# Kernel tuning notes

Hardware: AMD Instinct MI355X
Metric: run time of the kernel (lower is better)

## Reference

```python
import jax, jax.numpy as jnp
import numpy as np

B = 256                       # graphs in batch
NS = [4096, 2048, 1024, 512]  # nodes per graph at each stage (pool halves)
F_IN = 3                      # num_feature
D = 64                        # dim_cell
EPB = [32768, 16384, 8192]    # edges per graph at each layer (deg ~8)
NEG = 0.2                     # GATConv leaky_relu negative slope
EPS = 1e-5                    # BatchNorm eps
L = 3                         # layer_cell


def setup_inputs() -> dict:
    key = jax.random.key(0)
    ks = jax.random.split(key, 16)
    inp = {"x": jax.random.normal(ks[0], (B * NS[0], F_IN), jnp.float32)}
    dims = [F_IN, D, D]
    for i in range(L):
        inp[f"W{i}"] = jax.random.normal(ks[1 + i], (dims[i], D), jnp.float32) / np.sqrt(dims[i]).astype(np.float32)
        inp[f"as{i}"] = jax.random.normal(ks[4 + i], (D,), jnp.float32) * 0.1
        inp[f"ad{i}"] = jax.random.normal(ks[7 + i], (D,), jnp.float32) * 0.1
        inp[f"b{i}"] = jnp.zeros((D,), jnp.float32)
        inp[f"e{i}"] = jax.random.randint(ks[10 + i], (2, EPB[i]), 0, NS[i], jnp.int32)
        # cluster assignment: merge node pairs -> every cluster id occupied
        inp[f"c{i}"] = (jnp.arange(NS[i], dtype=jnp.int32) // 2)
    return inp


def _tile_edges(edge, n_per_graph):
    # replicate per-graph edge list across batch with node offsets, then add self-loops
    offs = (jnp.arange(B, dtype=edge.dtype) * n_per_graph)
    e = (edge[:, None, :] + offs[None, :, None]).reshape(2, -1)  # [2, B*E]
    loops = jnp.arange(B * n_per_graph, dtype=edge.dtype)
    return jnp.concatenate([e, jnp.stack([loops, loops])], axis=1)


def _gat(x, W, a_src, a_dst, bias, edge, n_tot):
    # PyG GATConv, heads=1: shared linear, edge-softmax over incoming edges
    h = x @ W                                # [n_tot, D]
    al_s = h @ a_src                         # [n_tot]
    al_d = h @ a_dst
    src, dst = edge[0], edge[1]              # message src j -> target i
    e = jax.nn.leaky_relu(al_s[src] + al_d[dst], NEG)
    m = jax.ops.segment_max(e, dst, num_segments=n_tot)
    ex = jnp.exp(e - m[dst])
    z = jax.ops.segment_sum(ex, dst, num_segments=n_tot)
    alpha = ex / z[dst]                      # softmax per target node
    out = jax.ops.segment_sum(alpha[:, None] * h[src], dst, num_segments=n_tot)
    return out + bias


def reference(x, W0, as0, ad0, b0, W1, as1, ad1, b1, W2, as2, ad2, b2,
              e0, e1, e2, c0, c1, c2):
    Ws, As, Ad, Bs = [W0, W1, W2], [as0, as1, as2], [ad0, ad1, ad2], [b0, b1, b2]
    Es, Cs = [e0, e1, e2], [c0, c1, c2]
    h = x
    for i in range(L):
        n_tot = B * NS[i]
        edge = _tile_edges(Es[i], NS[i])
        h = jax.nn.relu(_gat(h, Ws[i], As[i], Ad[i], Bs[i], edge, n_tot))
        # cluster max_pool: scatter-max nodes into clusters, offset per graph
        c_out = NS[i + 1]
        seg = (Cs[i][None, :] + (jnp.arange(B, dtype=jnp.int32) * c_out)[:, None]).reshape(-1)
        h = jax.ops.segment_max(h, seg, num_segments=B * c_out)
        # BatchNorm1d(affine=False), training-mode batch statistics
        h = (h - h.mean(axis=0)) * jax.lax.rsqrt(h.var(axis=0) + EPS)
    return h.reshape(B, NS[L] * D)
```

## Files before the change

kernel.cpp:

```cpp
#include <hip/hip_runtime.h>
#include <stdint.h>

#define NEG_SLOPE 0.2f
#define BN_EPS 1e-5f

typedef unsigned short u16;
typedef unsigned int   u32;
typedef __attribute__((ext_vector_type(2))) float  v2f;
typedef __attribute__((ext_vector_type(4))) float  f32x4;
typedef __attribute__((ext_vector_type(8))) short  short8;

__device__ __forceinline__ float lrelu(float x){ return fmaxf(x, NEG_SLOPE*x); }
__device__ __forceinline__ float bf2f(u16 u){ return __uint_as_float(((u32)u) << 16); }
__device__ __forceinline__ u16 f2bf(float f){
  u32 u = __float_as_uint(f);
  return (u16)((u + 0x7fffu + ((u >> 16) & 1u)) >> 16);
}

__global__ __launch_bounds__(256) void init_k(int* __restrict__ counts, u16* __restrict__ s0,
                                              u16* __restrict__ s1, u16* __restrict__ s2,
                                              int nc, int n0, int n1, int n2){
  int t = blockIdx.x*256 + threadIdx.x;
  int y = blockIdx.y;
  if (y==0){ if (t<nc) counts[t]=0; }
  else {
    u16* sd = (y==1)?s0:(y==2)?s1:s2;
    int n   = (y==1)?n0:(y==2)?n1:n2;
    if (t<n) sd[t]=0xFFFFu;
  }
}

__global__ __launch_bounds__(256) void hist_all_k(const int* __restrict__ el0, const int* __restrict__ el1,
                                                  const int* __restrict__ el2, int* __restrict__ c0,
                                                  int* __restrict__ c1, int* __restrict__ c2,
                                                  int n0, int n1, int n2){
  int t = blockIdx.x*256 + threadIdx.x;
  int L = blockIdx.y;
  const int* dst = (L==0)?(el0+n0):(L==1)?(el1+n1):(el2+n2);
  int* counts    = (L==0)?c0:(L==1)?c1:c2;
  int n          = (L==0)?n0:(L==1)?n1:n2;
  if (t < n) atomicAdd(&counts[dst[t]], 1);
}

__global__ __launch_bounds__(1024) void scan_all_k(int* __restrict__ c0, int* __restrict__ c1, int* __restrict__ c2,
                         int* __restrict__ ip0, int* __restrict__ ip1, int* __restrict__ ip2,
                         int* __restrict__ cu0, int* __restrict__ cu1, int* __restrict__ cu2,
                         u16* __restrict__ sd0, u16* __restrict__ sd1, u16* __restrict__ sd2,
                         int n0, int n1, int n2){
  int L = blockIdx.x;
  const int* counts = (L==0)?c0:(L==1)?c1:c2;
  int* indptr2      = (L==0)?ip0:(L==1)?ip1:ip2;
  int* cursor       = (L==0)?cu0:(L==1)?cu1:cu2;
  u16* ell_src      = (L==0)?sd0:(L==1)?sd1:sd2;
  int n             = (L==0)?n0:(L==1)?n1:n2;
  __shared__ int part[1024];
  int tid = threadIdx.x;
  int base = tid*4;
  int v0=0,v1=0,v2=0,v3=0;
  if (base+0<n) v0 = (counts[base+0]+4)&~3;
  if (base+1<n) v1 = (counts[base+1]+4)&~3;
  if (base+2<n) v2 = (counts[base+2]+4)&~3;
  if (base+3<n) v3 = (counts[base+3]+4)&~3;
  part[tid] = v0+v1+v2+v3;
  __syncthreads();
  for (int off=1; off<1024; off<<=1){
    int t2 = (tid>=off)?part[tid-off]:0;
    __syncthreads();
    part[tid] += t2;
    __syncthreads();
  }
  int run = (tid>0)?part[tid-1]:0;
  if (base+0<n){ indptr2[base+0]=run; cursor[base+0]=run+1; ell_src[run]=(u16)(base+0); run+=v0; }
  if (base+1<n){ indptr2[base+1]=run; cursor[base+1]=run+1; ell_src[run]=(u16)(base+1); run+=v1; }
  if (base+2<n){ indptr2[base+2]=run; cursor[base+2]=run+1; ell_src[run]=(u16)(base+2); run+=v2; }
  if (base+3<n){ indptr2[base+3]=run; cursor[base+3]=run+1; ell_src[run]=(u16)(base+3); run+=v3; }
  if (tid==0) indptr2[n] = part[1023];
}

__global__ __launch_bounds__(256) void scatter_all_k(const int* __restrict__ el0, const int* __restrict__ el1,
                         const int* __restrict__ el2, int* __restrict__ cu0, int* __restrict__ cu1,
                         int* __restrict__ cu2, u16* __restrict__ sd0, u16* __restrict__ sd1,
                         u16* __restrict__ sd2, int n0, int n1, int n2){
  int t = blockIdx.x*256 + threadIdx.x;
  int L = blockIdx.y;
  const int* el = (L==0)?el0:(L==1)?el1:el2;
  int* cursor   = (L==0)?cu0:(L==1)?cu1:cu2;
  u16* ell_src  = (L==0)?sd0:(L==1)?sd1:sd2;
  int n         = (L==0)?n0:(L==1)?n1:n2;
  if (t < n){
    int dd = el[n + t];
    int p = atomicAdd(&cursor[dd], 1);
    ell_src[p] = (u16)el[t];
  }
}

__global__ __launch_bounds__(1024) void pairsort_k(const int* __restrict__ c0, const int* __restrict__ c1,
                         const int* __restrict__ c2, u16* __restrict__ pm0, u16* __restrict__ pm1,
                         u16* __restrict__ pm2, int np0, int np1, int np2){
  int L = blockIdx.x;
  const int* counts = (L==0)?c0:(L==1)?c1:c2;
  u16* perm = (L==0)?pm0:(L==1)?pm1:pm2;
  int np    = (L==0)?np0:(L==1)?np1:np2;
  __shared__ int hist[64];
  __shared__ int pos[64];
  int t = threadIdx.x;
  if (t < 64) hist[t] = 0;
  __syncthreads();
  for (int p=t; p<np; p+=1024){
    int k = min(max(counts[2*p], counts[2*p+1]), 63);
    atomicAdd(&hist[k], 1);
  }
  __syncthreads();
  if (t == 0){ int run=0; for (int i=0;i<64;i++){ pos[i]=run; run+=hist[i]; } }
  __syncthreads();
  for (int p=t; p<np; p+=1024){
    int k = min(max(counts[2*p], counts[2*p+1]), 63);
    int q = atomicAdd(&pos[k], 1);
    perm[q] = (u16)p;
  }
}

__global__ __launch_bounds__(256) void gemm3_k(const float* __restrict__ x, const float* __restrict__ Wg,
                        const float* __restrict__ asrc, const float* __restrict__ adst,
                        u16* __restrict__ h, float* __restrict__ als, float* __restrict__ ald, int nrows8)
{
  const int l = threadIdx.x & 63;
  const int g = l >> 3;
  const int o = l & 7;
  float W0[8], W1[8], W2[8];
  float vs0=0.f,vs1=0.f,vs2=0.f,vd0=0.f,vd1=0.f,vd2=0.f;
  #pragma unroll
  for (int j=0;j<8;j++){
    W0[j] = Wg[      o*8 + j];
    W1[j] = Wg[ 64 + o*8 + j];
    W2[j] = Wg[128 + o*8 + j];
    float as = asrc[o*8 + j], ad = adst[o*8 + j];
    vs0 = fmaf(W0[j], as, vs0); vs1 = fmaf(W1[j], as, vs1); vs2 = fmaf(W2[j], as, vs2);
    vd0 = fmaf(W0[j], ad, vd0); vd1 = fmaf(W1[j], ad, vd1); vd2 = fmaf(W2[j], ad, vd2);
  }
  #pragma unroll
  for (int off=1; off<8; off<<=1){
    vs0 += __shfl_xor(vs0,off); vs1 += __shfl_xor(vs1,off); vs2 += __shfl_xor(vs2,off);
    vd0 += __shfl_xor(vd0,off); vd1 += __shfl_xor(vd1,off); vd2 += __shfl_xor(vd2,off);
  }
  int wv = blockIdx.x*4 + (int)(threadIdx.x>>6);
  int stride = gridDim.x*4;
  for (int blk = wv; blk < nrows8; blk += stride){
    int r = blk*8 + g;
    float x0 = x[(size_t)r*3+0];
    float x1 = x[(size_t)r*3+1];
    float x2 = x[(size_t)r*3+2];
    u32 pk[4];
    #pragma unroll
    for (int j=0;j<8;j+=2){
      float a0 = fmaf(x0, W0[j],   fmaf(x1, W1[j],   x2*W2[j]));
      float a1 = fmaf(x0, W0[j+1], fmaf(x1, W1[j+1], x2*W2[j+1]));
      pk[j>>1] = (u32)f2bf(a0) | ((u32)f2bf(a1) << 16);
    }
    ((int4*)(h + ((size_t)r << 6)))[o] = make_int4((int)pk[0],(int)pk[1],(int)pk[2],(int)pk[3]);
    if (o == 0){
      als[r] = fmaf(x2, vs2, fmaf(x1, vs1, x0*vs0));
      ald[r] = fmaf(x2, vd2, fmaf(x1, vd1, x0*vd0));
    }
  }
}

__global__ __launch_bounds__(128) void prep_w_k(const float* __restrict__ W, const float* __restrict__ asrc,
                        const float* __restrict__ adst, const float* __restrict__ scratch, float invN,
                        u16* __restrict__ wswz, float* __restrict__ cvec){
  __shared__ float mean_s[64], rstd_s[64], vs_s[64], vd_s[64], cv_s[64], acc[128];
  int t = threadIdx.x;
  float s = 0.f;
  #pragma unroll 8
  for (int b2=0;b2<256;b2++) s += scratch[b2*128 + t];
  acc[t] = s;
  __syncthreads();
  if (t < 64){
    float m = acc[t]*invN;
    float var = acc[64+t]*invN - m*m;
    mean_s[t] = m; rstd_s[t] = rsqrtf(var + BN_EPS);
  }
  __syncthreads();
  if (t < 64){
    float c = 0.f;
    for (int k=0;k<64;k++) c = fmaf(mean_s[k]*rstd_s[k], W[k*64+t], c);
    cv_s[t] = c; cvec[t] = c;
    float vs = 0.f, vd = 0.f;
    for (int col=0; col<64; col++){
      float wv = W[t*64+col];
      vs = fmaf(wv, asrc[col], vs);
      vd = fmaf(wv, adst[col], vd);
    }
    vs_s[t] = rstd_s[t]*vs; vd_s[t] = rstd_s[t]*vd;
  }
  __syncthreads();
  if (t == 0){
    float cs=0.f, cd=0.f;
    for (int col=0; col<64; col++){ cs = fmaf(cv_s[col], asrc[col], cs); cd = fmaf(cv_s[col], adst[col], cd); }
    cvec[64] = cs; cvec[65] = cd;
  }
  if (t < 64){
    #pragma unroll
    for (int f=0; f<8; f++){
      int tt = f >> 1, ch = f & 1;
      #pragma unroll
      for (int j=0; j<8; j++){
        int k   = ch*32 + (t>>4)*8 + j;
        int col = tt*16 + (t&15);
        wswz[(f*64 + t)*8 + j] = f2bf(rstd_s[k] * W[k*64 + col]);
      }
    }
    #pragma unroll
    for (int f=8; f<10; f++){
      int ch = f - 8;
      #pragma unroll
      for (int j=0; j<8; j++){
        int k = ch*32 + (t>>4)*8 + j;
        int colp = t & 15;
        float val = (colp==0)? vs_s[k] : (colp==1)? vd_s[k] : 0.f;
        wswz[(f*64 + t)*8 + j] = f2bf(val);
      }
    }
  }
}

__global__ __launch_bounds__(256) void gemm64_mfma_k(const u16* __restrict__ Pin, const u16* __restrict__ wswz,
                        const float* __restrict__ cvec,
                        u16* __restrict__ h, float* __restrict__ als, float* __restrict__ ald, int nblk16)
{
  const int l = threadIdx.x & 63;
  const int q = l >> 4;
  const int c = l & 15;
  short8 B[10];
  const int4* wsw = (const int4*)wswz;
  #pragma unroll
  for (int f=0; f<10; f++){
    int4 v = wsw[f*64 + l];
    B[f] = *(short8*)&v;
  }
  float cl[4];
  #pragma unroll
  for (int t=0;t<4;t++) cl[t] = cvec[t*16+c];
  const float const_s = cvec[64], const_d = cvec[65];
  int gw = blockIdx.x*4 + (int)(threadIdx.x>>6);
  int stride = gridDim.x*4;
  for (int blk = gw; blk < nblk16; blk += stride){
    size_t rowbase = (size_t)blk*16;
    const int4* arow = (const int4*)(Pin + (rowbase + c)*64);
    int4 a0v = arow[q];
    int4 a1v = arow[4+q];
    short8 A0 = *(short8*)&a0v, A1 = *(short8*)&a1v;
    f32x4 C0={0.f,0.f,0.f,0.f}, C1=C0, C2=C0, C3=C0, C4=C0;
    C0 = __builtin_amdgcn_mfma_f32_16x16x32_bf16(A0, B[0], C0, 0,0,0);
    C0 = __builtin_amdgcn_mfma_f32_16x16x32_bf16(A1, B[1], C0, 0,0,0);
    C1 = __builtin_amdgcn_mfma_f32_16x16x32_bf16(A0, B[2], C1, 0,0,0);
    C1 = __builtin_amdgcn_mfma_f32_16x16x32_bf16(A1, B[3], C1, 0,0,0);
    C2 = __builtin_amdgcn_mfma_f32_16x16x32_bf16(A0, B[4], C2, 0,0,0);
    C2 = __builtin_amdgcn_mfma_f32_16x16x32_bf16(A1, B[5], C2, 0,0,0);
    C3 = __builtin_amdgcn_mfma_f32_16x16x32_bf16(A0, B[6], C3, 0,0,0);
    C3 = __builtin_amdgcn_mfma_f32_16x16x32_bf16(A1, B[7], C3, 0,0,0);
    C4 = __builtin_amdgcn_mfma_f32_16x16x32_bf16(A0, B[8], C4, 0,0,0);
    C4 = __builtin_amdgcn_mfma_f32_16x16x32_bf16(A1, B[9], C4, 0,0,0);
    #pragma unroll
    for (int t=0;t<4;t++){
      f32x4 C = (t==0)?C0:(t==1)?C1:(t==2)?C2:C3;
      #pragma unroll
      for (int reg=0;reg<4;reg++){
        h[(rowbase + q*4 + reg)*64 + t*16 + c] = f2bf(C[reg] - cl[t]);
      }
    }
    if (c == 0){
      #pragma unroll
      for (int reg=0;reg<4;reg++) als[rowbase + q*4 + reg] = C4[reg] - const_s;
    } else if (c == 1){
      #pragma unroll
      for (int reg=0;reg<4;reg++) ald[rowbase + q*4 + reg] = C4[reg] - const_d;
    }
  }
}

__global__ __launch_bounds__(256) void gat_pool_k(const u16* __restrict__ h, const float* __restrict__ bias,
                      const int* __restrict__ indptr2, const int* __restrict__ counts,
                      const u16* __restrict__ perm, const u16* __restrict__ ell_src,
                      const float* __restrict__ als, const float* __restrict__ ald,
                      u16* __restrict__ P, int log2NS, int nwaves)
{
  const int l = threadIdx.x & 63;
  const int g = l >> 3;
  const int o = l & 7;
  const int NB  = gridDim.x;
  const int bid = blockIdx.x;
  const int lb  = (bid & 7) * (NB >> 3) + (bid >> 3);
  const int wv  = lb * 4 + (int)(threadIdx.x >> 6);
  if (wv >= nwaves) return;

  const int wbits = log2NS - 3;
  const int b    = wv >> wbits;
  const int widx = wv & ((1 << wbits) - 1);
  const int pairslot = widx*4 + (g >> 1);
  const int prow = perm[pairslot];
  const int d = 2*prow + (g & 1);
  const int nmask = (1 << log2NS) - 1;
  const int base = b << log2NS;
  const u32* hb = (const u32*)(h + ((size_t)base << 6)) + (o << 2);
  const float* alsg = als + base;

  const int p0  = indptr2[d];
  const int cnt = counts[d] + 1;
  const float ald_d = ald[base + d];

  const float* bp = bias + (o << 3);
  float4 bA = *(const float4*)(bp);
  float4 bB = *(const float4*)(bp + 4);

  v2f a01={0.f,0.f}, a23={0.f,0.f}, a45={0.f,0.f}, a67={0.f,0.f};
  float z = 0.f;

  int m0 = ell_src[p0];
  int m1 = ell_src[p0+1];
  int m2 = ell_src[p0+2];
  int s0i = m0 & nmask;
  const u32* hp0 = hb + ((size_t)s0i << 5);
  u32 h00=hp0[0], h01=hp0[1], h02=hp0[2], h03=hp0[3];
  float al0 = alsg[s0i];
  int s1i = m1 & nmask;
  const u32* hp1 = hb + ((size_t)s1i << 5);
  u32 h10=hp1[0], h11=hp1[1], h12=hp1[2], h13=hp1[3];
  float al1 = alsg[s1i];

  for (int it = 0; it < cnt; ++it){
    int s2i = m2 & nmask;
    const u32* hp2 = hb + ((size_t)s2i << 5);
    u32 n0=hp2[0], n1=hp2[1], n2=hp2[2], n3=hp2[3];
    float al2 = alsg[s2i];
    int m3 = ell_src[p0 + it + 3];
    float w = (m0 == 0xFFFF) ? 0.f : __expf(lrelu(al0 + ald_d));
    z += w;
    v2f w2 = {w, w};
    a01 += (v2f){ __uint_as_float(h00 << 16), __uint_as_float(h00 & 0xffff0000u) } * w2;
    a23 += (v2f){ __uint_as_float(h01 << 16), __uint_as_float(h01 & 0xffff0000u) } * w2;
    a45 += (v2f){ __uint_as_float(h02 << 16), __uint_as_float(h02 & 0xffff0000u) } * w2;
    a67 += (v2f){ __uint_as_float(h03 << 16), __uint_as_float(h03 & 0xffff0000u) } * w2;
    m0 = m1; m1 = m2; m2 = m3;
    h00=h10; h01=h11; h02=h12; h03=h13; al0 = al1;
    h10=n0;  h11=n1;  h12=n2;  h13=n3;  al1 = al2;
  }

  float rz = __builtin_amdgcn_rcpf(z);
  float q0 = fmaxf(fmaf(a01.x, rz, bA.x), 0.f);
  float q1 = fmaxf(fmaf(a01.y, rz, bA.y), 0.f);
  float q2 = fmaxf(fmaf(a23.x, rz, bA.z), 0.f);
  float q3 = fmaxf(fmaf(a23.y, rz, bA.w), 0.f);
  float q4 = fmaxf(fmaf(a45.x, rz, bB.x), 0.f);
  float q5 = fmaxf(fmaf(a45.y, rz, bB.y), 0.f);
  float q6 = fmaxf(fmaf(a67.x, rz, bB.z), 0.f);
  float q7 = fmaxf(fmaf(a67.y, rz, bB.w), 0.f);
  q0 = fmaxf(q0, __shfl_xor(q0, 8));
  q1 = fmaxf(q1, __shfl_xor(q1, 8));
  q2 = fmaxf(q2, __shfl_xor(q2, 8));
  q3 = fmaxf(q3, __shfl_xor(q3, 8));
  q4 = fmaxf(q4, __shfl_xor(q4, 8));
  q5 = fmaxf(q5, __shfl_xor(q5, 8));
  q6 = fmaxf(q6, __shfl_xor(q6, 8));
  q7 = fmaxf(q7, __shfl_xor(q7, 8));
  if ((g & 1) == 0){
    u32 w0 = (u32)f2bf(q0) | ((u32)f2bf(q1) << 16);
    u32 w1 = (u32)f2bf(q2) | ((u32)f2bf(q3) << 16);
    u32 w2p = (u32)f2bf(q4) | ((u32)f2bf(q5) << 16);
    u32 w3 = (u32)f2bf(q6) | ((u32)f2bf(q7) << 16);
    size_t prowg = ((size_t)b << (log2NS - 1)) + prow;
    ((int4*)(P + (prowg << 6)))[o] = make_int4((int)w0,(int)w1,(int)w2p,(int)w3);
  }
}

__global__ __launch_bounds__(256) void bn_stats_k(const u16* __restrict__ P, float* __restrict__ scratch, int iters){
  const int l = threadIdx.x & 63;
  int gw = blockIdx.x*4 + (threadIdx.x>>6);
  int GW = gridDim.x*4;
  float s = 0.f, s2 = 0.f;
  #pragma unroll 4
  for (int i = 0; i < iters; i++){
    int r = gw + i*GW;
    float v = bf2f(P[(size_t)r*64 + l]);
    s += v; s2 = fmaf(v, v, s2);
  }
  __shared__ float ls[256], ls2[256];
  ls[threadIdx.x] = s; ls2[threadIdx.x] = s2;
  __syncthreads();
  if (threadIdx.x < 64){
    float S  = ls[threadIdx.x] + ls[threadIdx.x+64] + ls[threadIdx.x+128] + ls[threadIdx.x+192];
    float S2 = ls2[threadIdx.x] + ls2[threadIdx.x+64] + ls2[threadIdx.x+128] + ls2[threadIdx.x+192];
    scratch[blockIdx.x*128 + threadIdx.x] = S;
    scratch[blockIdx.x*128 + 64 + threadIdx.x] = S2;
  }
}

__global__ __launch_bounds__(128) void bn_finish_k(const float* __restrict__ scratch, float* __restrict__ stats,
                                                   int nblocks, float invN){
  __shared__ float accs[128];
  int j = threadIdx.x;
  float s = 0.f;
  #pragma unroll 8
  for (int b=0;b<nblocks;b++) s += scratch[b*128 + j];
  accs[j] = s;
  __syncthreads();
  if (j < 64){
    float m = accs[j]*invN;
    float var = accs[j+64]*invN - m*m;
    stats[j] = m;
    stats[64+j] = rsqrtf(var + BN_EPS);
  }
}

__global__ __launch_bounds__(256) void bn_apply_k(const u32* __restrict__ P2, const float* __restrict__ stats,
                                                  float4* __restrict__ out, int nq){
  int t = blockIdx.x*256 + threadIdx.x;
  if (t >= nq) return;
  int l = (t*4) & 63;
  u32 v0 = P2[t*2], v1 = P2[t*2+1];
  float4 r;
  r.x = (__uint_as_float((v0 & 0xffffu) << 16) - stats[l+0]) * stats[64+l+0];
  r.y = (__uint_as_float( v0 & 0xffff0000u    ) - stats[l+1]) * stats[64+l+1];
  r.z = (__uint_as_float((v1 & 0xffffu) << 16) - stats[l+2]) * stats[64+l+2];
  r.w = (__uint_as_float( v1 & 0xffff0000u    ) - stats[l+3]) * stats[64+l+3];
  out[t] = r;
}

extern "C" void kernel_launch(void* const* d_in, const int* in_sizes, int n_in,
                              void* d_out, int out_size, void* d_ws, size_t ws_size,
                              hipStream_t stream)
{
  const float* x      = (const float*)d_in[0];
  const float* Wl[3]  = {(const float*)d_in[1], (const float*)d_in[7],  (const float*)d_in[13]};
  const float* asl[3] = {(const float*)d_in[2], (const float*)d_in[8],  (const float*)d_in[14]};
  const float* adl[3] = {(const float*)d_in[3], (const float*)d_in[9],  (const float*)d_in[15]};
  const float* bl[3]  = {(const float*)d_in[4], (const float*)d_in[10], (const float*)d_in[16]};
  const int*   el[3]  = {(const int*)d_in[5],   (const int*)d_in[11],   (const int*)d_in[17]};

  const int NS[4]  = {4096, 2048, 1024, 512};
  const int EPB[3] = {32768, 16384, 8192};
  const int LOG2NS[3] = {12, 11, 10};
  const int ECAP[3] = {32768+4*4096, 16384+4*2048, 8192+4*1024};
  const int BATCH = 256;

  char* ws = (char*)d_ws;
  size_t off = 0;
  auto alloc = [&](size_t bytes)->char*{
    char* p = ws + off; off += (bytes + 255) & ~(size_t)255; return p;
  };

  u16*   hbuf    = (u16*)alloc((size_t)BATCH*NS[0]*64*2);
  u16*   Pbuf    = (u16*)alloc((size_t)BATCH*NS[1]*64*2);
  float* als     = (float*)alloc((size_t)BATCH*NS[0]*4);
  float* ald     = (float*)alloc((size_t)BATCH*NS[0]*4);
  float* scratch = (float*)alloc(256*128*4);
  float* stats   = (float*)alloc(128*4);
  u16*   wswz    = (u16*)alloc(10*64*8*2);
  float* cvec    = (float*)alloc(128*4);
  int* counts_all = (int*)alloc((size_t)(NS[0]+NS[1]+NS[2])*4);
  int* cursor_all = (int*)alloc((size_t)(NS[0]+NS[1]+NS[2])*4);
  int *counts[3], *cursor[3], *indptr2[3];
  u16* ell_src[3];
  u16* perm[3];
  counts[0]=counts_all; counts[1]=counts_all+NS[0]; counts[2]=counts_all+NS[0]+NS[1];
  cursor[0]=cursor_all; cursor[1]=cursor_all+NS[0]; cursor[2]=cursor_all+NS[0]+NS[1];
  for (int i=0;i<3;i++){
    indptr2[i] = (int*)alloc((size_t)(NS[i]+1)*4);
    ell_src[i] = (u16*)alloc((size_t)(ECAP[i]+16)*2);
    perm[i]    = (u16*)alloc((size_t)NS[i]);
  }
  if (off > ws_size) return;

  int ctot = NS[0]+NS[1]+NS[2];
  {
    dim3 ginit((ECAP[0]+16+255)/256, 4);
    init_k<<<ginit, 256, 0, stream>>>(counts_all, ell_src[0], ell_src[1], ell_src[2],
                                      ctot, ECAP[0]+16, ECAP[1]+16, ECAP[2]+16);
    dim3 ghist(EPB[0]/256, 3);
    hist_all_k<<<ghist, 256, 0, stream>>>(el[0], el[1], el[2], counts[0], counts[1], counts[2],
                                          EPB[0], EPB[1], EPB[2]);
    scan_all_k<<<3, 1024, 0, stream>>>(counts[0], counts[1], counts[2],
                                       indptr2[0], indptr2[1], indptr2[2],
                                       cursor[0], cursor[1], cursor[2],
                                       ell_src[0], ell_src[1], ell_src[2],
                                       NS[0], NS[1], NS[2]);
    scatter_all_k<<<ghist, 256, 0, stream>>>(el[0], el[1], el[2],
                                             cursor[0], cursor[1], cursor[2],
                                             ell_src[0], ell_src[1], ell_src[2],
                                             EPB[0], EPB[1], EPB[2]);
    pairsort_k<<<3, 1024, 0, stream>>>(counts[0], counts[1], counts[2],
                                       perm[0], perm[1], perm[2],
                                       NS[0]/2, NS[1]/2, NS[2]/2);
  }

  for (int i=0;i<3;i++){
    int ntot = BATCH*NS[i];

    if (i==0){
      gemm3_k<<<1024, 256, 0, stream>>>(x, Wl[0], asl[0], adl[0], hbuf, als, ald, ntot/8);
    } else {
      float invN = 1.0f / (float)(BATCH*NS[i]);
      prep_w_k<<<1, 128, 0, stream>>>(Wl[i], asl[i], adl[i], scratch, invN, wswz, cvec);
      gemm64_mfma_k<<<2048, 256, 0, stream>>>(Pbuf, wswz, cvec, hbuf, als, ald, ntot/16);
    }

    int nwaves = ntot/8;
    gat_pool_k<<<nwaves/4, 256, 0, stream>>>(hbuf, bl[i], indptr2[i], counts[i], perm[i],
                                             ell_src[i], als, ald,
                                             Pbuf, LOG2NS[i], nwaves);

    bn_stats_k<<<256, 256, 0, stream>>>(Pbuf, scratch, (ntot/2)/1024);
  }

  bn_finish_k<<<1, 128, 0, stream>>>(scratch, stats, 256, 1.0f/(float)(BATCH*NS[3]));
  int nq = out_size/4;
  bn_apply_k<<<(nq+255)/256, 256, 0, stream>>>((const u32*)Pbuf, stats, (float4*)d_out, nq);
}
```

Baseline: 550.9 us.

## Switch to node-major batch-interleaved layout so GAT waves share graph structure

Result: slower. 578.9 us (+5.1%).

```diff
diff --git a/kernel.cpp b/kernel.cpp
--- a/kernel.cpp
+++ b/kernel.cpp
@@ -94,35 +94,9 @@
   }
 }
 
-__global__ __launch_bounds__(1024) void pairsort_k(const int* __restrict__ c0, const int* __restrict__ c1,
-                         const int* __restrict__ c2, u16* __restrict__ pm0, u16* __restrict__ pm1,
-                         u16* __restrict__ pm2, int np0, int np1, int np2){
-  int L = blockIdx.x;
-  const int* counts = (L==0)?c0:(L==1)?c1:c2;
-  u16* perm = (L==0)?pm0:(L==1)?pm1:pm2;
-  int np    = (L==0)?np0:(L==1)?np1:np2;
-  __shared__ int hist[64];
-  __shared__ int pos[64];
-  int t = threadIdx.x;
-  if (t < 64) hist[t] = 0;
-  __syncthreads();
-  for (int p=t; p<np; p+=1024){
-    int k = min(max(counts[2*p], counts[2*p+1]), 63);
-    atomicAdd(&hist[k], 1);
-  }
-  __syncthreads();
-  if (t == 0){ int run=0; for (int i=0;i<64;i++){ pos[i]=run; run+=hist[i]; } }
-  __syncthreads();
-  for (int p=t; p<np; p+=1024){
-    int k = min(max(counts[2*p], counts[2*p+1]), 63);
-    int q = atomicAdd(&pos[k], 1);
-    perm[q] = (u16)p;
-  }
-}
-
 __global__ __launch_bounds__(256) void gemm3_k(const float* __restrict__ x, const float* __restrict__ Wg,
                         const float* __restrict__ asrc, const float* __restrict__ adst,
-                        u16* __restrict__ h, float* __restrict__ als, float* __restrict__ ald, int nrows8)
+                        u16* __restrict__ h, float* __restrict__ als, float* __restrict__ ald, int nunits)
 {
   const int l = threadIdx.x & 63;
   const int g = l >> 3;
@@ -145,11 +119,13 @@
   }
   int wv = blockIdx.x*4 + (int)(threadIdx.x>>6);
   int stride = gridDim.x*4;
-  for (int blk = wv; blk < nrows8; blk += stride){
-    int r = blk*8 + g;
-    float x0 = x[(size_t)r*3+0];
-    float x1 = x[(size_t)r*3+1];
-    float x2 = x[(size_t)r*3+2];
+  for (int u = wv; u < nunits; u += stride){
+    int b = u & 255;
+    int n = ((u >> 8) << 3) + g;
+    float x0 = x[(size_t)(b*4096 + n)*3 + 0];
+    float x1 = x[(size_t)(b*4096 + n)*3 + 1];
+    float x2 = x[(size_t)(b*4096 + n)*3 + 2];
+    size_t r = (size_t)n*256 + b;
     u32 pk[4];
     #pragma unroll
     for (int j=0;j<8;j+=2){
@@ -157,7 +133,7 @@
       float a1 = fmaf(x0, W0[j+1], fmaf(x1, W1[j+1], x2*W2[j+1]));
       pk[j>>1] = (u32)f2bf(a0) | ((u32)f2bf(a1) << 16);
     }
-    ((int4*)(h + ((size_t)r << 6)))[o] = make_int4((int)pk[0],(int)pk[1],(int)pk[2],(int)pk[3]);
+    ((int4*)(h + (r << 6)))[o] = make_int4((int)pk[0],(int)pk[1],(int)pk[2],(int)pk[3]);
     if (o == 0){
       als[r] = fmaf(x2, vs2, fmaf(x1, vs1, x0*vs0));
       ald[r] = fmaf(x2, vd2, fmaf(x1, vd1, x0*vd0));
@@ -281,96 +257,102 @@
 
 __global__ __launch_bounds__(256) void gat_pool_k(const u16* __restrict__ h, const float* __restrict__ bias,
                       const int* __restrict__ indptr2, const int* __restrict__ counts,
-                      const u16* __restrict__ perm, const u16* __restrict__ ell_src,
+                      const u16* __restrict__ ell_src,
                       const float* __restrict__ als, const float* __restrict__ ald,
-                      u16* __restrict__ P, int log2NS, int nwaves)
+                      u16* __restrict__ P, int log2NS)
 {
   const int l = threadIdx.x & 63;
-  const int g = l >> 3;
+  const int b_off = l >> 3;
   const int o = l & 7;
-  const int NB  = gridDim.x;
+  const int wv = threadIdx.x >> 6;
   const int bid = blockIdx.x;
-  const int lb  = (bid & 7) * (NB >> 3) + (bid >> 3);
-  const int wv  = lb * 4 + (int)(threadIdx.x >> 6);
-  if (wv >= nwaves) return;
-
-  const int wbits = log2NS - 3;
-  const int b    = wv >> wbits;
-  const int widx = wv & ((1 << wbits) - 1);
-  const int pairslot = widx*4 + (g >> 1);
-  const int prow = perm[pairslot];
-  const int d = 2*prow + (g & 1);
+  const int log2bpc = log2NS - 3;
+  const int c = (bid & 7) | (((bid >> (3 + log2bpc)) & 3) << 3);
+  const int within = (bid >> 3) & ((1 << log2bpc) - 1);
+  const int pair = within*4 + wv;
+  const int bg = c*8 + b_off;
+  const int laneoff = bg*64 + o*8;
   const int nmask = (1 << log2NS) - 1;
-  const int base = b << log2NS;
-  const u32* hb = (const u32*)(h + ((size_t)base << 6)) + (o << 2);
-  const float* alsg = als + base;
-
-  const int p0  = indptr2[d];
-  const int cnt = counts[d] + 1;
-  const float ald_d = ald[base + d];
-
-  const float* bp = bias + (o << 3);
-  float4 bA = *(const float4*)(bp);
-  float4 bB = *(const float4*)(bp + 4);
-
-  v2f a01={0.f,0.f}, a23={0.f,0.f}, a45={0.f,0.f}, a67={0.f,0.f};
-  float z = 0.f;
-
-  int m0 = ell_src[p0];
-  int m1 = ell_src[p0+1];
-  int m2 = ell_src[p0+2];
-  int s0i = m0 & nmask;
-  const u32* hp0 = hb + ((size_t)s0i << 5);
-  u32 h00=hp0[0], h01=hp0[1], h02=hp0[2], h03=hp0[3];
-  float al0 = alsg[s0i];
-  int s1i = m1 & nmask;
-  const u32* hp1 = hb + ((size_t)s1i << 5);
-  u32 h10=hp1[0], h11=hp1[1], h12=hp1[2], h13=hp1[3];
-  float al1 = alsg[s1i];
-
-  for (int it = 0; it < cnt; ++it){
-    int s2i = m2 & nmask;
-    const u32* hp2 = hb + ((size_t)s2i << 5);
-    u32 n0=hp2[0], n1=hp2[1], n2=hp2[2], n3=hp2[3];
-    float al2 = alsg[s2i];
-    int m3 = ell_src[p0 + it + 3];
-    float w = (m0 == 0xFFFF) ? 0.f : __expf(lrelu(al0 + ald_d));
-    z += w;
-    v2f w2 = {w, w};
-    a01 += (v2f){ __uint_as_float(h00 << 16), __uint_as_float(h00 & 0xffff0000u) } * w2;
-    a23 += (v2f){ __uint_as_float(h01 << 16), __uint_as_float(h01 & 0xffff0000u) } * w2;
-    a45 += (v2f){ __uint_as_float(h02 << 16), __uint_as_float(h02 & 0xffff0000u) } * w2;
-    a67 += (v2f){ __uint_as_float(h03 << 16), __uint_as_float(h03 & 0xffff0000u) } * w2;
-    m0 = m1; m1 = m2; m2 = m3;
-    h00=h10; h01=h11; h02=h12; h03=h13; al0 = al1;
-    h10=n0;  h11=n1;  h12=n2;  h13=n3;  al1 = al2;
-  }
-
-  float rz = __builtin_amdgcn_rcpf(z);
-  float q0 = fmaxf(fmaf(a01.x, rz, bA.x), 0.f);
-  float q1 = fmaxf(fmaf(a01.y, rz, bA.y), 0.f);
-  float q2 = fmaxf(fmaf(a23.x, rz, bA.z), 0.f);
-  float q3 = fmaxf(fmaf(a23.y, rz, bA.w), 0.f);
-  float q4 = fmaxf(fmaf(a45.x, rz, bB.x), 0.f);
-  float q5 = fmaxf(fmaf(a45.y, rz, bB.y), 0.f);
-  float q6 = fmaxf(fmaf(a67.x, rz, bB.z), 0.f);
-  float q7 = fmaxf(fmaf(a67.y, rz, bB.w), 0.f);
-  q0 = fmaxf(q0, __shfl_xor(q0, 8));
-  q1 = fmaxf(q1, __shfl_xor(q1, 8));
-  q2 = fmaxf(q2, __shfl_xor(q2, 8));
-  q3 = fmaxf(q3, __shfl_xor(q3, 8));
-  q4 = fmaxf(q4, __shfl_xor(q4, 8));
-  q5 = fmaxf(q5, __shfl_xor(q5, 8));
-  q6 = fmaxf(q6, __shfl_xor(q6, 8));
-  q7 = fmaxf(q7, __shfl_xor(q7, 8));
-  if ((g & 1) == 0){
-    u32 w0 = (u32)f2bf(q0) | ((u32)f2bf(q1) << 16);
-    u32 w1 = (u32)f2bf(q2) | ((u32)f2bf(q3) << 16);
-    u32 w2p = (u32)f2bf(q4) | ((u32)f2bf(q5) << 16);
-    u32 w3 = (u32)f2bf(q6) | ((u32)f2bf(q7) << 16);
-    size_t prowg = ((size_t)b << (log2NS - 1)) + prow;
-    ((int4*)(P + (prowg << 6)))[o] = make_int4((int)w0,(int)w1,(int)w2p,(int)w3);
-  }
+
+  float q[8];
+  #pragma unroll
+  for (int j=0;j<8;j++) q[j] = 0.f;
+
+  #pragma unroll
+  for (int dd=0; dd<2; dd++){
+    const int d = 2*pair + dd;
+    const int p0 = indptr2[d];
+    const int cnt = counts[d] + 1;
+    const float ald_d = ald[(size_t)d*256 + bg];
+
+    v2f a01={0.f,0.f}, a23={0.f,0.f}, a45={0.f,0.f}, a67={0.f,0.f};
+    float z = 0.f;
+
+    int mA = ell_src[p0] & nmask;
+    int4 hA = *(const int4*)(h + (((size_t)mA) << 14) + laneoff);
+    float aA = als[(size_t)mA*256 + bg];
+    int mB = ell_src[p0+1] & nmask;
+    int4 hB = *(const int4*)(h + (((size_t)mB) << 14) + laneoff);
+    float aB = als[(size_t)mB*256 + bg];
+
+    int it = 0;
+    while (it + 1 < cnt){
+      {
+        float w = __expf(lrelu(aA + ald_d));
+        z += w;
+        v2f w2 = {w, w};
+        u32 r0=((u32*)&hA)[0], r1=((u32*)&hA)[1], r2=((u32*)&hA)[2], r3=((u32*)&hA)[3];
+        a01 += (v2f){ __uint_as_float(r0 << 16), __uint_as_float(r0 & 0xffff0000u) } * w2;
+        a23 += (v2f){ __uint_as_float(r1 << 16), __uint_as_float(r1 & 0xffff0000u) } * w2;
+        a45 += (v2f){ __uint_as_float(r2 << 16), __uint_as_float(r2 & 0xffff0000u) } * w2;
+        a67 += (v2f){ __uint_as_float(r3 << 16), __uint_as_float(r3 & 0xffff0000u) } * w2;
+      }
+      mA = ell_src[p0 + it + 2] & nmask;
+      hA = *(const int4*)(h + (((size_t)mA) << 14) + laneoff);
+      aA = als[(size_t)mA*256 + bg];
+      {
+        float w = __expf(lrelu(aB + ald_d));
+        z += w;
+        v2f w2 = {w, w};
+        u32 r0=((u32*)&hB)[0], r1=((u32*)&hB)[1], r2=((u32*)&hB)[2], r3=((u32*)&hB)[3];
+        a01 += (v2f){ __uint_as_float(r0 << 16), __uint_as_float(r0 & 0xffff0000u) } * w2;
+        a23 += (v2f){ __uint_as_float(r1 << 16), __uint_as_float(r1 & 0xffff0000u) } * w2;
+        a45 += (v2f){ __uint_as_float(r2 << 16), __uint_as_float(r2 & 0xffff0000u) } * w2;
+        a67 += (v2f){ __uint_as_float(r3 << 16), __uint_as_float(r3 & 0xffff0000u) } * w2;
+      }
+      mB = ell_src[p0 + it + 3] & nmask;
+      hB = *(const int4*)(h + (((size_t)mB) << 14) + laneoff);
+      aB = als[(size_t)mB*256 + bg];
+      it += 2;
+    }
+    if (it < cnt){
+      float w = __expf(lrelu(aA + ald_d));
+      z += w;
+      v2f w2 = {w, w};
+      u32 r0=((u32*)&hA)[0], r1=((u32*)&hA)[1], r2=((u32*)&hA)[2], r3=((u32*)&hA)[3];
+      a01 += (v2f){ __uint_as_float(r0 << 16), __uint_as_float(r0 & 0xffff0000u) } * w2;
+      a23 += (v2f){ __uint_as_float(r1 << 16), __uint_as_float(r1 & 0xffff0000u) } * w2;
+      a45 += (v2f){ __uint_as_float(r2 << 16), __uint_as_float(r2 & 0xffff0000u) } * w2;
+      a67 += (v2f){ __uint_as_float(r3 << 16), __uint_as_float(r3 & 0xffff0000u) } * w2;
+    }
+
+    float rz = __builtin_amdgcn_rcpf(z);
+    const float* bp = bias + o*8;
+    q[0] = fmaxf(q[0], fmaxf(fmaf(a01.x, rz, bp[0]), 0.f));
+    q[1] = fmaxf(q[1], fmaxf(fmaf(a01.y, rz, bp[1]), 0.f));
+    q[2] = fmaxf(q[2], fmaxf(fmaf(a23.x, rz, bp[2]), 0.f));
+    q[3] = fmaxf(q[3], fmaxf(fmaf(a23.y, rz, bp[3]), 0.f));
+    q[4] = fmaxf(q[4], fmaxf(fmaf(a45.x, rz, bp[4]), 0.f));
+    q[5] = fmaxf(q[5], fmaxf(fmaf(a45.y, rz, bp[5]), 0.f));
+    q[6] = fmaxf(q[6], fmaxf(fmaf(a67.x, rz, bp[6]), 0.f));
+    q[7] = fmaxf(q[7], fmaxf(fmaf(a67.y, rz, bp[7]), 0.f));
+  }
+
+  u32 w0 = (u32)f2bf(q[0]) | ((u32)f2bf(q[1]) << 16);
+  u32 w1 = (u32)f2bf(q[2]) | ((u32)f2bf(q[3]) << 16);
+  u32 w2p = (u32)f2bf(q[4]) | ((u32)f2bf(q[5]) << 16);
+  u32 w3 = (u32)f2bf(q[6]) | ((u32)f2bf(q[7]) << 16);
+  ((int4*)(P + (((size_t)pair*256 + bg) << 6)))[o] = make_int4((int)w0,(int)w1,(int)w2p,(int)w3);
 }
 
 __global__ __launch_bounds__(256) void bn_stats_k(const u16* __restrict__ P, float* __restrict__ scratch, int iters){
@@ -412,18 +394,31 @@
   }
 }
 
-__global__ __launch_bounds__(256) void bn_apply_k(const u32* __restrict__ P2, const float* __restrict__ stats,
-                                                  float4* __restrict__ out, int nq){
-  int t = blockIdx.x*256 + threadIdx.x;
-  if (t >= nq) return;
-  int l = (t*4) & 63;
-  u32 v0 = P2[t*2], v1 = P2[t*2+1];
-  float4 r;
-  r.x = (__uint_as_float((v0 & 0xffffu) << 16) - stats[l+0]) * stats[64+l+0];
-  r.y = (__uint_as_float( v0 & 0xffff0000u    ) - stats[l+1]) * stats[64+l+1];
-  r.z = (__uint_as_float((v1 & 0xffffu) << 16) - stats[l+2]) * stats[64+l+2];
-  r.w = (__uint_as_float( v1 & 0xffff0000u    ) - stats[l+3]) * stats[64+l+3];
-  out[t] = r;
+__global__ __launch_bounds__(256) void bn_apply_k(const u16* __restrict__ P, const float* __restrict__ stats,
+                                                  float* __restrict__ out, int nunits){
+  int u = blockIdx.x*4 + (int)(threadIdx.x>>6);
+  if (u >= nunits) return;
+  const int l = threadIdx.x & 63;
+  const int b_off = l >> 3;
+  const int o = l & 7;
+  int c = u & 31, n = u >> 5;
+  int bg = c*8 + b_off;
+  int4 v = *(const int4*)(P + (((size_t)n*256 + bg) << 6) + o*8);
+  u32 r0=((u32*)&v)[0], r1=((u32*)&v)[1], r2=((u32*)&v)[2], r3=((u32*)&v)[3];
+  const float* mp = stats + o*8;
+  const float* rp = stats + 64 + o*8;
+  float4 f0, f1;
+  f0.x = (__uint_as_float(r0 << 16)          - mp[0]) * rp[0];
+  f0.y = (__uint_as_float(r0 & 0xffff0000u)  - mp[1]) * rp[1];
+  f0.z = (__uint_as_float(r1 << 16)          - mp[2]) * rp[2];
+  f0.w = (__uint_as_float(r1 & 0xffff0000u)  - mp[3]) * rp[3];
+  f1.x = (__uint_as_float(r2 << 16)          - mp[4]) * rp[4];
+  f1.y = (__uint_as_float(r2 & 0xffff0000u)  - mp[5]) * rp[5];
+  f1.z = (__uint_as_float(r3 << 16)          - mp[6]) * rp[6];
+  f1.w = (__uint_as_float(r3 & 0xffff0000u)  - mp[7]) * rp[7];
+  float* op = out + (size_t)bg*32768 + (size_t)n*64 + o*8;
+  *(float4*)(op)   = f0;
+  *(float4*)(op+4) = f1;
 }
 
 extern "C" void kernel_launch(void* const* d_in, const int* in_sizes, int n_in,
@@ -461,13 +456,11 @@
   int* cursor_all = (int*)alloc((size_t)(NS[0]+NS[1]+NS[2])*4);
   int *counts[3], *cursor[3], *indptr2[3];
   u16* ell_src[3];
-  u16* perm[3];
   counts[0]=counts_all; counts[1]=counts_all+NS[0]; counts[2]=counts_all+NS[0]+NS[1];
   cursor[0]=cursor_all; cursor[1]=cursor_all+NS[0]; cursor[2]=cursor_all+NS[0]+NS[1];
   for (int i=0;i<3;i++){
     indptr2[i] = (int*)alloc((size_t)(NS[i]+1)*4);
     ell_src[i] = (u16*)alloc((size_t)(ECAP[i]+16)*2);
-    perm[i]    = (u16*)alloc((size_t)NS[i]);
   }
   if (off > ws_size) return;
 
@@ -488,9 +481,6 @@
                                              cursor[0], cursor[1], cursor[2],
                                              ell_src[0], ell_src[1], ell_src[2],
                                              EPB[0], EPB[1], EPB[2]);
-    pairsort_k<<<3, 1024, 0, stream>>>(counts[0], counts[1], counts[2],
-                                       perm[0], perm[1], perm[2],
-                                       NS[0]/2, NS[1]/2, NS[2]/2);
   }
 
   for (int i=0;i<3;i++){
@@ -504,15 +494,14 @@
       gemm64_mfma_k<<<2048, 256, 0, stream>>>(Pbuf, wswz, cvec, hbuf, als, ald, ntot/16);
     }
 
-    int nwaves = ntot/8;
-    gat_pool_k<<<nwaves/4, 256, 0, stream>>>(hbuf, bl[i], indptr2[i], counts[i], perm[i],
-                                             ell_src[i], als, ald,
-                                             Pbuf, LOG2NS[i], nwaves);
+    int nblocks = 4 * NS[i];
+    gat_pool_k<<<nblocks, 256, 0, stream>>>(hbuf, bl[i], indptr2[i], counts[i],
+                                            ell_src[i], als, ald, Pbuf, LOG2NS[i]);
 
     bn_stats_k<<<256, 256, 0, stream>>>(Pbuf, scratch, (ntot/2)/1024);
   }
 
   bn_finish_k<<<1, 128, 0, stream>>>(scratch, stats, 256, 1.0f/(float)(BATCH*NS[3]));
-  int nq = out_size/4;
-  bn_apply_k<<<(nq+255)/256, 256, 0, stream>>>((const u32*)Pbuf, stats, (float4*)d_out, nq);
-}
+  int nunits = NS[3]*32;
+  bn_apply_k<<<nunits/4, 256, 0, stream>>>(Pbuf, stats, (float*)d_out, nunits);
+}
```
